# Performance work log

Hardware: AMD Instinct MI355X
Metric: run time of the kernel (lower is better)

## Reference

```python
import jax, jax.numpy as jnp
import numpy as np

E = 1024
H = 16
DH = E // H
FF = 4 * E
EPS = 1e-5


def _layer_norm(x, g, b):
    mu = jnp.mean(x, axis=-1, keepdims=True)
    var = jnp.var(x, axis=-1, keepdims=True)
    return (x - mu) * jax.lax.rsqrt(var + EPS) * g + b


def setup_inputs() -> dict:
    key = jax.random.key(0)
    ks = jax.random.split(key, 12)
    B, S = 2, 2048
    s_e = 1.0 / np.sqrt(E)
    s_f = 1.0 / np.sqrt(FF)
    return {
        "hidden_states": jax.random.normal(ks[0], (B, S, E), jnp.float32),
        "attention_mask": jnp.zeros((B, S), jnp.float32),
        "position_bias": jax.random.normal(ks[1], (H, S, S), jnp.float32) * 0.1,
        "Wq": jax.random.normal(ks[2], (E, E), jnp.float32) * s_e,
        "bq": jnp.zeros((E,), jnp.float32),
        "Wk": jax.random.normal(ks[3], (E, E), jnp.float32) * s_e,
        "bk": jnp.zeros((E,), jnp.float32),
        "Wv": jax.random.normal(ks[4], (E, E), jnp.float32) * s_e,
        "bv": jnp.zeros((E,), jnp.float32),
        "Wo": jax.random.normal(ks[5], (E, E), jnp.float32) * s_e,
        "bo": jnp.zeros((E,), jnp.float32),
        "ln1_g": jnp.ones((E,), jnp.float32),
        "ln1_b": jnp.zeros((E,), jnp.float32),
        "W1": jax.random.normal(ks[6], (E, FF), jnp.float32) * s_e,
        "b1": jnp.zeros((FF,), jnp.float32),
        "W2": jax.random.normal(ks[7], (FF, E), jnp.float32) * s_f,
        "b2": jnp.zeros((E,), jnp.float32),
        "ln2_g": jnp.ones((E,), jnp.float32),
        "ln2_b": jnp.zeros((E,), jnp.float32),
    }


def reference(hidden_states, attention_mask, position_bias, Wq, bq, Wk, bk, Wv, bv,
              Wo, bo, ln1_g, ln1_b, W1, b1, W2, b2, ln2_g, ln2_b):
    B, S, _ = hidden_states.shape
    x = hidden_states
    # QKV projections, split heads: [B, S, H, DH]
    q = (x @ Wq + bq).reshape(B, S, H, DH)
    k = (x @ Wk + bk).reshape(B, S, H, DH)
    v = (x @ Wv + bv).reshape(B, S, H, DH)
    # scores: [B, H, S, S]
    scores = jnp.einsum("bshd,bthd->bhst", q, k) / np.sqrt(DH).astype(np.float32)
    scores = scores + position_bias[None] + attention_mask[:, None, None, :]
    probs = jax.nn.softmax(scores, axis=-1)  # dropout is identity in eval
    ctx = jnp.einsum("bhst,bthd->bshd", probs, v).reshape(B, S, E)
    attn_out = ctx @ Wo + bo
    h = _layer_norm(x + attn_out, ln1_g, ln1_b)
    ffn = jax.nn.gelu(h @ W1 + b1, approximate=False) @ W2 + b2
    return _layer_norm(h + ffn, ln2_g, ln2_b)
```

## Files before the change

kernel.cpp:

```cpp
#include <hip/hip_runtime.h>
#include <stdint.h>

#define EDIM   1024
#define NHEAD  16
#define DHEAD  64
#define FFDIM  4096
#define SEQLEN 2048
#define NBATCH 2
#define MROWS  (NBATCH * SEQLEN)
#define NT     (SEQLEN / 64)

typedef __attribute__((ext_vector_type(8))) short bf16x8;
typedef __attribute__((ext_vector_type(4))) float f32x4;

static __device__ __forceinline__ unsigned short f2bf(float f) {
    union { float f; uint32_t u; } v; v.f = f;
    return (unsigned short)((v.u + 0x7fffu + ((v.u >> 16) & 1u)) >> 16);
}

static __device__ __forceinline__ void gload16(const void* g, void* s) {
    __builtin_amdgcn_global_load_lds(
        (const __attribute__((address_space(1))) unsigned int*)g,
        (__attribute__((address_space(3))) unsigned int*)s,
        16, 0, 0);
}

__global__ void k_cast_bf16(const float* __restrict__ in, unsigned short* __restrict__ out, int n4) {
    int i = blockIdx.x * blockDim.x + threadIdx.x;
    if (i < n4) {
        float4 v = ((const float4*)in)[i];
        ushort4 o;
        o.x = f2bf(v.x); o.y = f2bf(v.y); o.z = f2bf(v.z); o.w = f2bf(v.w);
        ((ushort4*)out)[i] = o;
    }
}

__global__ void k_transpose_cast(const float* __restrict__ in, unsigned short* __restrict__ out,
                                 int R, int C) {
    __shared__ float tile[32][33];
    int c0 = blockIdx.x * 32, r0 = blockIdx.y * 32;
    int tx = threadIdx.x, ty = threadIdx.y;
    #pragma unroll
    for (int i = 0; i < 32; i += 8)
        tile[ty + i][tx] = in[(size_t)(r0 + ty + i) * C + c0 + tx];
    __syncthreads();
    #pragma unroll
    for (int i = 0; i < 32; i += 8)
        out[(size_t)(c0 + ty + i) * R + r0 + tx] = f2bf(tile[tx][ty + i]);
}

__global__ void k_transpose_v(const unsigned short* __restrict__ V, int vstride,
                              unsigned short* __restrict__ Vt) {
    __shared__ unsigned short tile[32][33];
    const int bh = blockIdx.z, b = bh >> 4, h = bh & 15;
    const int s0 = blockIdx.x * 32, d0 = blockIdx.y * 32;
    const int tx = threadIdx.x, ty = threadIdx.y;
    #pragma unroll
    for (int i = 0; i < 32; i += 8)
        tile[ty + i][tx] = V[(size_t)(b * SEQLEN + s0 + ty + i) * vstride + h * DHEAD + d0 + tx];
    __syncthreads();
    #pragma unroll
    for (int i = 0; i < 32; i += 8)
        Vt[((size_t)(b * NHEAD + h) * DHEAD + d0 + ty + i) * SEQLEN + s0 + tx] = tile[tx][ty + i];
}

__global__ void k_concat_bias(const float* __restrict__ bq, const float* __restrict__ bk,
                              const float* __restrict__ bv, float* __restrict__ out) {
    int i = blockIdx.x * 256 + threadIdx.x;
    const float* src = (i < 1024) ? bq : (i < 2048) ? bk : bv;
    out[i] = src[i & 1023];
}

template <int TBM, int TBN, int EPI, int SPLITK>
__global__ __launch_bounds__(256, 2) void k_gemm(
    const unsigned short* __restrict__ A,
    const unsigned short* __restrict__ Bt,
    const float* __restrict__ bias,
    void* __restrict__ Cout, int M, int N, int K)
{
    constexpr int MR = TBM / 32, NR = TBN / 32;
    __shared__ __attribute__((aligned(16))) unsigned short Asm[TBM * 64];
    __shared__ __attribute__((aligned(16))) unsigned short Bsm[TBN * 64];

    const int nbx = gridDim.x;
    const int flat = blockIdx.y * nbx + blockIdx.x;
    const int cpx = (nbx * gridDim.y) >> 3;
    const int swz = (flat & 7) * cpx + (flat >> 3);
    const int bx = swz % nbx, by = swz / nbx;
    const int kz = (SPLITK > 1) ? blockIdx.z : 0;
    const int Ksub = K / SPLITK;

    const int row0 = by * TBM, col0 = bx * TBN;
    const int t = threadIdx.x;
    const int lane = t & 63, w = t >> 6;
    const int wm = w >> 1, wn = w & 1;
    const int l15 = lane & 15, l4 = lane >> 4;
    const int sr = lane >> 3, sc = (lane & 7) * 8;

    f32x4 acc[MR][NR];
    #pragma unroll
    for (int m = 0; m < MR; ++m)
        #pragma unroll
        for (int n = 0; n < NR; ++n) acc[m][n] = (f32x4){0.f, 0.f, 0.f, 0.f};

    for (int k0 = kz * Ksub; k0 < (kz + 1) * Ksub; k0 += 64) {
        #pragma unroll
        for (int i = 0; i < TBM / 32; ++i) {
            const int r = w * (TBM / 4) + i * 8;
            gload16(A + (size_t)(row0 + r + sr) * K + k0 + sc, &Asm[r * 64]);
        }
        #pragma unroll
        for (int i = 0; i < TBN / 32; ++i) {
            const int r = w * (TBN / 4) + i * 8;
            gload16(Bt + (size_t)(col0 + r + sr) * K + k0 + sc, &Bsm[r * 64]);
        }
        __syncthreads();
        #pragma unroll
        for (int kk = 0; kk < 64; kk += 32) {
            bf16x8 af[MR], bf[NR];
            #pragma unroll
            for (int m = 0; m < MR; ++m)
                af[m] = *(const bf16x8*)&Asm[(wm * (TBM / 2) + m * 16 + l15) * 64 + kk + l4 * 8];
            #pragma unroll
            for (int n = 0; n < NR; ++n)
                bf[n] = *(const bf16x8*)&Bsm[(wn * (TBN / 2) + n * 16 + l15) * 64 + kk + l4 * 8];
            #pragma unroll
            for (int m = 0; m < MR; ++m)
                #pragma unroll
                for (int n = 0; n < NR; ++n)
                    acc[m][n] = __builtin_amdgcn_mfma_f32_16x16x32_bf16(af[m], bf[n], acc[m][n], 0, 0, 0);
        }
        __syncthreads();
    }

    #pragma unroll
    for (int m = 0; m < MR; ++m) {
        int rb = row0 + wm * (TBM / 2) + m * 16 + l4 * 4;
        #pragma unroll
        for (int n = 0; n < NR; ++n) {
            int c = col0 + wn * (TBN / 2) + n * 16 + l15;
            float bv = (SPLITK == 1 || kz == 0) ? bias[c] : 0.0f;
            #pragma unroll
            for (int i = 0; i < 4; ++i) {
                float v = acc[m][n][i] + bv;
                if (EPI == 1) v = 0.5f * v * (1.0f + erff(v * 0.70710678118654752f));
                if (EPI == 2) {
                    float* outp = (float*)Cout + (size_t)kz * M * N;
                    outp[(size_t)(rb + i) * N + c] = v;
                } else {
                    ((unsigned short*)Cout)[(size_t)(rb + i) * N + c] = f2bf(v);
                }
            }
        }
    }
}

__global__ __launch_bounds__(512, 2) void k_attn(
    const unsigned short* __restrict__ QKV,
    const unsigned short* __restrict__ Vt,
    const float* __restrict__ pbias,
    const float* __restrict__ mask,
    unsigned short* __restrict__ Ctx)
{
    __shared__ __attribute__((aligned(16))) unsigned short Ksm[2][2][64 * 64];
    __shared__ __attribute__((aligned(16))) unsigned short Vsm[2][2][64 * 64];
    __shared__ __attribute__((aligned(16))) unsigned short Psm[8][16 * 32];

    const int flat = blockIdx.x;
    const int swz = (flat & 7) * 64 + (flat >> 3);
    const int qt = swz & 31;
    const int h  = swz >> 5;

    const int t = threadIdx.x;
    const int lane = t & 63, w = t >> 6;
    const int wb = w & 1;
    const int wq = (w >> 1) * 16;
    const int l15 = lane & 15, l4 = lane >> 4;
    const int qrow = qt * 64 + wq;

    const float* pbrow = pbias + ((size_t)h * SEQLEN + qrow + l4 * 4) * SEQLEN;
    const float* mrow  = mask + wb * SEQLEN;

    bf16x8 qf0, qf1;
    {
        const unsigned short* qp = QKV + (size_t)(wb * SEQLEN + qrow + l15) * (3 * EDIM) + h * DHEAD + l4 * 8;
        bf16x8 r0 = *(const bf16x8*)qp;
        bf16x8 r1 = *(const bf16x8*)(qp + 32);
        #pragma unroll
        for (int e = 0; e < 8; ++e) {
            union { uint32_t u; float f; } c0, c1;
            c0.u = (uint32_t)(unsigned short)r0[e] << 16;
            c1.u = (uint32_t)(unsigned short)r1[e] << 16;
            r0[e] = (short)f2bf(c0.f * 0.125f);
            r1[e] = (short)f2bf(c1.f * 0.125f);
        }
        qf0 = r0; qf1 = r1;
    }

    f32x4 oacc[4];
    #pragma unroll
    for (int nd = 0; nd < 4; ++nd) oacc[nd] = (f32x4){0.f, 0.f, 0.f, 0.f};
    float m_run[4] = {-1e30f, -1e30f, -1e30f, -1e30f};
    float l_run[4] = {0.f, 0.f, 0.f, 0.f};

    const int srow = lane >> 3;
    const int schk = lane & 7;
    const int r7 = l15 & 7;

    auto stage = [&](int buf, int kt) {
        const int kbase = kt * 64;
        #pragma unroll
        for (int j = 0; j < 4; ++j) {
            const int q  = w * 4 + j;
            const int kv = q >> 4;
            const int bb = (q >> 3) & 1;
            const int g  = q & 7;
            const int row = g * 8 + srow;
            const int cg  = (schk ^ (row & 7)) * 8;
            if (kv == 0)
                gload16(QKV + (size_t)(bb * SEQLEN + kbase + row) * (3 * EDIM) + EDIM + h * DHEAD + cg,
                        &Ksm[buf][bb][g * 512]);
            else
                gload16(Vt + ((size_t)((bb * NHEAD + h) * DHEAD) + row) * SEQLEN + kbase + cg,
                        &Vsm[buf][bb][g * 512]);
        }
    };

    auto compute = [&](int buf, int kt) {
        const int kbase = kt * 64;
        float p[4][4];
        float tmax[4] = {-1e30f, -1e30f, -1e30f, -1e30f};
        #pragma unroll
        for (int n = 0; n < 4; ++n) {
            const int scol = kbase + n * 16 + l15;
            const float mk = mrow[scol];
            f32x4 z;
            #pragma unroll
            for (int i = 0; i < 4; ++i) z[i] = pbrow[(size_t)i * SEQLEN + scol] + mk;
            bf16x8 kb0 = *(const bf16x8*)&Ksm[buf][wb][(n * 16 + l15) * 64 + ((l4 ^ r7) << 3)];
            bf16x8 kb1 = *(const bf16x8*)&Ksm[buf][wb][(n * 16 + l15) * 64 + (((4 + l4) ^ r7) << 3)];
            z = __builtin_amdgcn_mfma_f32_16x16x32_bf16(qf0, kb0, z, 0, 0, 0);
            z = __builtin_amdgcn_mfma_f32_16x16x32_bf16(qf1, kb1, z, 0, 0, 0);
            #pragma unroll
            for (int i = 0; i < 4; ++i) {
                p[n][i] = z[i];
                tmax[i] = fmaxf(tmax[i], z[i]);
            }
        }
        #pragma unroll
        for (int i = 0; i < 4; ++i) {
            float mv = tmax[i];
            #pragma unroll
            for (int off = 1; off < 16; off <<= 1) mv = fmaxf(mv, __shfl_xor(mv, off, 64));
            float mnew = fmaxf(m_run[i], mv);
            float alpha = __expf(m_run[i] - mnew);
            m_run[i] = mnew;
            float sum = 0.f;
            #pragma unroll
            for (int n = 0; n < 4; ++n) { p[n][i] = __expf(p[n][i] - mnew); sum += p[n][i]; }
            #pragma unroll
            for (int off = 1; off < 16; off <<= 1) sum += __shfl_xor(sum, off, 64);
            l_run[i] = l_run[i] * alpha + sum;
            #pragma unroll
            for (int nd = 0; nd < 4; ++nd) oacc[nd][i] *= alpha;
        }
        #pragma unroll
        for (int hh = 0; hh < 2; ++hh) {
            #pragma unroll
            for (int n = 0; n < 2; ++n)
                #pragma unroll
                for (int i = 0; i < 4; ++i) {
                    const int row = l4 * 4 + i;
                    const int cl = n * 16 + l15;
                    Psm[w][row * 32 + (((cl >> 3) ^ (row & 3)) << 3) + (cl & 7)] =
                        f2bf(p[2 * hh + n][i]);
                }
            bf16x8 pa = *(const bf16x8*)&Psm[w][l15 * 32 + ((l4 ^ (l15 & 3)) << 3)];
            #pragma unroll
            for (int nd = 0; nd < 4; ++nd) {
                bf16x8 vf = *(const bf16x8*)&Vsm[buf][wb][(nd * 16 + l15) * 64 + (((hh * 4 + l4) ^ r7) << 3)];
                oacc[nd] = __builtin_amdgcn_mfma_f32_16x16x32_bf16(pa, vf, oacc[nd], 0, 0, 0);
            }
        }
    };

    stage(0, 0);
    __syncthreads();
    int buf = 0;
    for (int kt = 0; kt < NT; ++kt) {
        stage(buf ^ 1, (kt + 1) & (NT - 1));
        compute(buf, kt);
        __syncthreads();
        buf ^= 1;
    }

    #pragma unroll
    for (int nd = 0; nd < 4; ++nd)
        #pragma unroll
        for (int i = 0; i < 4; ++i) {
            float v = oacc[nd][i] / l_run[i];
            Ctx[(size_t)(wb * SEQLEN + qrow + l4 * 4 + i) * EDIM + h * DHEAD + nd * 16 + l15] = f2bf(v);
        }
}

template <int WRITE_BF>
__global__ __launch_bounds__(256) void k_ln(
    const float* __restrict__ X, const float* __restrict__ T, const float* __restrict__ T2,
    const float* __restrict__ gam, const float* __restrict__ bet,
    float* __restrict__ Of, unsigned short* __restrict__ Ob)
{
    const int r = blockIdx.x;
    const int t = threadIdx.x;
    const size_t base = (size_t)r * EDIM + t * 4;
    float4 xv = *(const float4*)(X + base);
    float4 tv = *(const float4*)(T + base);
    float4 t2 = *(const float4*)(T2 + base);
    float4 s = make_float4(xv.x + tv.x + t2.x, xv.y + tv.y + t2.y,
                           xv.z + tv.z + t2.z, xv.w + tv.w + t2.w);
    float sum = s.x + s.y + s.z + s.w;
    float sq  = s.x * s.x + s.y * s.y + s.z * s.z + s.w * s.w;
    #pragma unroll
    for (int off = 1; off < 64; off <<= 1) {
        sum += __shfl_xor(sum, off, 64);
        sq  += __shfl_xor(sq,  off, 64);
    }
    __shared__ float red[8];
    const int lane = t & 63, w = t >> 6;
    if (lane == 0) { red[w] = sum; red[4 + w] = sq; }
    __syncthreads();
    sum = red[0] + red[1] + red[2] + red[3];
    sq  = red[4] + red[5] + red[6] + red[7];
    const float mu = sum * (1.0f / EDIM);
    const float var = sq * (1.0f / EDIM) - mu * mu;
    const float rs = rsqrtf(var + 1e-5f);
    float4 gv = *(const float4*)(gam + t * 4);
    float4 bv = *(const float4*)(bet + t * 4);
    float4 o = make_float4((s.x - mu) * rs * gv.x + bv.x,
                           (s.y - mu) * rs * gv.y + bv.y,
                           (s.z - mu) * rs * gv.z + bv.z,
                           (s.w - mu) * rs * gv.w + bv.w);
    *(float4*)(Of + base) = o;
    if (WRITE_BF) {
        ushort4 ob;
        ob.x = f2bf(o.x); ob.y = f2bf(o.y); ob.z = f2bf(o.z); ob.w = f2bf(o.w);
        *(ushort4*)(Ob + base) = ob;
    }
}

extern "C" void kernel_launch(void* const* d_in, const int* in_sizes, int n_in,
                              void* d_out, int out_size, void* d_ws, size_t ws_size,
                              hipStream_t stream) {
    const float* x    = (const float*)d_in[0];
    const float* mask = (const float*)d_in[1];
    const float* pb   = (const float*)d_in[2];
    const float* Wq = (const float*)d_in[3];  const float* bq = (const float*)d_in[4];
    const float* Wk = (const float*)d_in[5];  const float* bk = (const float*)d_in[6];
    const float* Wv = (const float*)d_in[7];  const float* bv = (const float*)d_in[8];
    const float* Wo = (const float*)d_in[9];  const float* bo = (const float*)d_in[10];
    const float* g1 = (const float*)d_in[11]; const float* be1 = (const float*)d_in[12];
    const float* W1 = (const float*)d_in[13]; const float* b1 = (const float*)d_in[14];
    const float* W2 = (const float*)d_in[15]; const float* b2 = (const float*)d_in[16];
    const float* g2 = (const float*)d_in[17]; const float* be2 = (const float*)d_in[18];
    float* out = (float*)d_out;

    char* ws = (char*)d_ws;
    const size_t MB = 1024 * 1024;
    unsigned short* qkv  = (unsigned short*)(ws + 0);
    unsigned short* gbf  = (unsigned short*)(ws + 0);
    unsigned short* wqt  = (unsigned short*)(ws + 32 * MB);
    unsigned short* wkt  = (unsigned short*)(ws + 34 * MB);
    unsigned short* wvt  = (unsigned short*)(ws + 36 * MB);
    unsigned short* wot  = (unsigned short*)(ws + 38 * MB);
    unsigned short* w1t  = (unsigned short*)(ws + 40 * MB);
    unsigned short* w2t  = (unsigned short*)(ws + 48 * MB);
    float*          bcat = (float*)(ws + 56 * MB);
    unsigned short* ctxb = (unsigned short*)(ws + 56 * MB);
    unsigned short* xb   = (unsigned short*)(ws + 64 * MB);
    unsigned short* vt   = (unsigned short*)(ws + 64 * MB);
    float*          pt0  = (float*)(ws + 72 * MB);
    float*          pt1  = (float*)(ws + 88 * MB);
    float*          hf   = (float*)(ws + 104 * MB);
    unsigned short* hb   = (unsigned short*)(ws + 120 * MB);

    const dim3 b256(256);
    const dim3 tb(32, 8);

    k_cast_bf16<<<dim3(MROWS * EDIM / 4 / 256), b256, 0, stream>>>(x, xb, MROWS * EDIM / 4);
    k_transpose_cast<<<dim3(EDIM / 32, EDIM / 32), tb, 0, stream>>>(Wq, wqt, EDIM, EDIM);
    k_transpose_cast<<<dim3(EDIM / 32, EDIM / 32), tb, 0, stream>>>(Wk, wkt, EDIM, EDIM);
    k_transpose_cast<<<dim3(EDIM / 32, EDIM / 32), tb, 0, stream>>>(Wv, wvt, EDIM, EDIM);
    k_transpose_cast<<<dim3(EDIM / 32, EDIM / 32), tb, 0, stream>>>(Wo, wot, EDIM, EDIM);
    k_transpose_cast<<<dim3(FFDIM / 32, EDIM / 32), tb, 0, stream>>>(W1, w1t, EDIM, FFDIM);
    k_transpose_cast<<<dim3(EDIM / 32, FFDIM / 32), tb, 0, stream>>>(W2, w2t, FFDIM, EDIM);
    k_concat_bias<<<dim3(12), b256, 0, stream>>>(bq, bk, bv, bcat);

    k_gemm<128, 128, 0, 1><<<dim3(3 * EDIM / 128, MROWS / 128), b256, 0, stream>>>(
        xb, wqt, bcat, qkv, MROWS, 3 * EDIM, EDIM);
    k_transpose_v<<<dim3(SEQLEN / 32, DHEAD / 32, NBATCH * NHEAD), tb, 0, stream>>>(
        qkv + 2 * EDIM, 3 * EDIM, vt);

    k_attn<<<dim3(512), dim3(512), 0, stream>>>(qkv, vt, pb, mask, ctxb);

    k_gemm<128, 128, 2, 2><<<dim3(EDIM / 128, MROWS / 128, 2), b256, 0, stream>>>(
        ctxb, wot, bo, pt0, MROWS, EDIM, EDIM);
    k_ln<1><<<dim3(MROWS), b256, 0, stream>>>(x, pt0, pt1, g1, be1, hf, hb);
    k_gemm<128, 128, 1, 1><<<dim3(FFDIM / 128, MROWS / 128), b256, 0, stream>>>(
        hb, w1t, b1, gbf, MROWS, FFDIM, EDIM);
    k_gemm<128, 128, 2, 2><<<dim3(EDIM / 128, MROWS / 128, 2), b256, 0, stream>>>(
        gbf, w2t, b2, pt0, MROWS, EDIM, FFDIM);
    k_ln<0><<<dim3(MROWS), b256, 0, stream>>>(hf, pt0, pt1, g2, be2, out, nullptr);
    (void)in_sizes; (void)n_in; (void)out_size; (void)ws_size;
}
```

Before: 368.7 us.

## Prefetch position-bias tiles one step ahead in attention and batch weight transposes

In the attention kernel, the position-bias and mask loads for the next key tile are issued into registers alongside the LDS stage of that tile, so they overlap with the current tile's MFMA work instead of stalling it. The main loop is unrolled by two with fixed buffer indices and ping-pong register sets. Separately, the four square weight transpose-casts are merged into one launch over a z-dimension to save launch overhead. The prefetch doubles the registers held for bias values, which may lower occupancy of the 512-thread attention blocks.

```diff
diff --git a/kernel.cpp b/kernel.cpp
--- a/kernel.cpp
+++ b/kernel.cpp
@@ -47,6 +47,25 @@
     #pragma unroll
     for (int i = 0; i < 32; i += 8)
         out[(size_t)(c0 + ty + i) * R + r0 + tx] = f2bf(tile[tx][ty + i]);
+}
+
+__global__ void k_transpose_cast4(const float* __restrict__ s0, const float* __restrict__ s1,
+                                  const float* __restrict__ s2, const float* __restrict__ s3,
+                                  unsigned short* __restrict__ d0, unsigned short* __restrict__ d1,
+                                  unsigned short* __restrict__ d2, unsigned short* __restrict__ d3) {
+    __shared__ float tile[32][33];
+    const int z = blockIdx.z;
+    const float* in = (z == 0) ? s0 : (z == 1) ? s1 : (z == 2) ? s2 : s3;
+    unsigned short* out = (z == 0) ? d0 : (z == 1) ? d1 : (z == 2) ? d2 : d3;
+    int c0 = blockIdx.x * 32, r0 = blockIdx.y * 32;
+    int tx = threadIdx.x, ty = threadIdx.y;
+    #pragma unroll
+    for (int i = 0; i < 32; i += 8)
+        tile[ty + i][tx] = in[(size_t)(r0 + ty + i) * EDIM + c0 + tx];
+    __syncthreads();
+    #pragma unroll
+    for (int i = 0; i < 32; i += 8)
+        out[(size_t)(c0 + ty + i) * EDIM + r0 + tx] = f2bf(tile[tx][ty + i]);
 }
 
 __global__ void k_transpose_v(const unsigned short* __restrict__ V, int vstride,
@@ -226,17 +245,24 @@
         }
     };
 
-    auto compute = [&](int buf, int kt) {
+    auto loadPB = [&](int kt, f32x4 (&pb)[4]) {
         const int kbase = kt * 64;
-        float p[4][4];
-        float tmax[4] = {-1e30f, -1e30f, -1e30f, -1e30f};
         #pragma unroll
         for (int n = 0; n < 4; ++n) {
             const int scol = kbase + n * 16 + l15;
             const float mk = mrow[scol];
-            f32x4 z;
-            #pragma unroll
-            for (int i = 0; i < 4; ++i) z[i] = pbrow[(size_t)i * SEQLEN + scol] + mk;
+            #pragma unroll
+            for (int i = 0; i < 4; ++i)
+                pb[n][i] = pbrow[(size_t)i * SEQLEN + scol] + mk;
+        }
+    };
+
+    auto compute = [&](int buf, const f32x4 (&pb)[4]) {
+        float p[4][4];
+        float tmax[4] = {-1e30f, -1e30f, -1e30f, -1e30f};
+        #pragma unroll
+        for (int n = 0; n < 4; ++n) {
+            f32x4 z = pb[n];
             bf16x8 kb0 = *(const bf16x8*)&Ksm[buf][wb][(n * 16 + l15) * 64 + ((l4 ^ r7) << 3)];
             bf16x8 kb1 = *(const bf16x8*)&Ksm[buf][wb][(n * 16 + l15) * 64 + (((4 + l4) ^ r7) << 3)];
             z = __builtin_amdgcn_mfma_f32_16x16x32_bf16(qf0, kb0, z, 0, 0, 0);
@@ -284,14 +310,20 @@
         }
     };
 
+    f32x4 pbA[4], pbB[4];
     stage(0, 0);
+    loadPB(0, pbA);
     __syncthreads();
-    int buf = 0;
-    for (int kt = 0; kt < NT; ++kt) {
-        stage(buf ^ 1, (kt + 1) & (NT - 1));
-        compute(buf, kt);
+
+    for (int kt = 0; kt < NT; kt += 2) {
+        stage(1, (kt + 1) & (NT - 1));
+        loadPB((kt + 1) & (NT - 1), pbB);
+        compute(0, pbA);
         __syncthreads();
-        buf ^= 1;
+        stage(0, (kt + 2) & (NT - 1));
+        loadPB((kt + 2) & (NT - 1), pbA);
+        compute(1, pbB);
+        __syncthreads();
     }
 
     #pragma unroll
@@ -386,10 +418,8 @@
     const dim3 tb(32, 8);
 
     k_cast_bf16<<<dim3(MROWS * EDIM / 4 / 256), b256, 0, stream>>>(x, xb, MROWS * EDIM / 4);
-    k_transpose_cast<<<dim3(EDIM / 32, EDIM / 32), tb, 0, stream>>>(Wq, wqt, EDIM, EDIM);
-    k_transpose_cast<<<dim3(EDIM / 32, EDIM / 32), tb, 0, stream>>>(Wk, wkt, EDIM, EDIM);
-    k_transpose_cast<<<dim3(EDIM / 32, EDIM / 32), tb, 0, stream>>>(Wv, wvt, EDIM, EDIM);
-    k_transpose_cast<<<dim3(EDIM / 32, EDIM / 32), tb, 0, stream>>>(Wo, wot, EDIM, EDIM);
+    k_transpose_cast4<<<dim3(EDIM / 32, EDIM / 32, 4), tb, 0, stream>>>(
+        Wq, Wk, Wv, Wo, wqt, wkt, wvt, wot);
     k_transpose_cast<<<dim3(FFDIM / 32, EDIM / 32), tb, 0, stream>>>(W1, w1t, EDIM, FFDIM);
     k_transpose_cast<<<dim3(EDIM / 32, FFDIM / 32), tb, 0, stream>>>(W2, w2t, FFDIM, EDIM);
     k_concat_bias<<<dim3(12), b256, 0, stream>>>(bq, bk, bv, bcat);
```

New measurement: 438.7 us. +19.0%, slower.
